# Kernel tuning notes

Hardware: AMD Instinct MI355X
Metric: run time of the kernel (lower is better)

The kernel has to match this reference:

```python
import jax, jax.numpy as jnp
import numpy as np

N_NODES = 100000
N_EDGES = 1600000
IN_C, HID_C, OUT_C = 256, 128, 64


def sage_conv(x, src, dst, Wl, Wr, b, n_nodes):
    """PyG SAGEConv: lin_l(mean of neighbor messages) + lin_r(x) + b."""
    msgs = x[src]  # [E, C] gather
    agg = jax.ops.segment_sum(msgs, dst, num_segments=n_nodes)  # [N, C] scatter-add
    deg = jax.ops.segment_sum(jnp.ones((src.shape[0],), x.dtype), dst, num_segments=n_nodes)
    agg = agg / jnp.maximum(deg, 1.0)[:, None]  # mean aggregation, safe for isolated nodes
    return agg @ Wl + x @ Wr + b


def setup_inputs() -> dict:
    key = jax.random.key(0)
    ks = jax.random.split(key, 12)

    def glorot(k, shape):
        fan_in, fan_out = shape
        lim = float(np.sqrt(6.0 / (fan_in + fan_out)))
        return jax.random.uniform(k, shape, jnp.float32, -lim, lim)

    x = jax.random.normal(ks[0], (N_NODES, IN_C), jnp.float32)
    edge_index = jax.random.randint(ks[1], (2, N_EDGES), 0, N_NODES, jnp.int32)
    return {
        "x": x,
        "edge_index": edge_index,
        "Wl0": glorot(ks[2], (IN_C, HID_C)),
        "Wr0": glorot(ks[3], (IN_C, HID_C)),
        "b0": jnp.zeros((HID_C,), jnp.float32),
        "Wl1": glorot(ks[4], (HID_C, HID_C)),
        "Wr1": glorot(ks[5], (HID_C, HID_C)),
        "b1": jnp.zeros((HID_C,), jnp.float32),
        "Wl2": glorot(ks[6], (HID_C, OUT_C)),
        "Wr2": glorot(ks[7], (HID_C, OUT_C)),
        "b2": jnp.zeros((OUT_C,), jnp.float32),
    }


def reference(x, edge_index, Wl0, Wr0, b0, Wl1, Wr1, b1, Wl2, Wr2, b2):
    src, dst = edge_index[0], edge_index[1]
    n = x.shape[0]
    h = x
    out = None
    # convs[:-1]: conv -> relu -> dropout (eval mode: dropout = identity)
    for Wl, Wr, b in ((Wl0, Wr0, b0), (Wl1, Wr1, b1)):
        out = sage_conv(h, src, dst, Wl, Wr, b, n)
        h = jax.nn.relu(out)
    g = h
    x_final = sage_conv(g, src, dst, Wl2, Wr2, b2, n)
    return (x_final, out, g)
```

## Files before the change

kernel.cpp:

```cpp
#include <hip/hip_runtime.h>
#include <stdint.h>

typedef __attribute__((ext_vector_type(4))) float f32x4;
typedef _Float16 half8 __attribute__((ext_vector_type(8)));
typedef _Float16 half4 __attribute__((ext_vector_type(4)));


#define BIN_CHUNK 8192
#define MAXB 512


template <int K, int NCOLT>
__device__ inline void wprep_one(const float* __restrict__ Wl, const float* __restrict__ Wr,
                                 _Float16* __restrict__ Wt, int i) {
    constexpr int NCOL = NCOLT / 2;
    int n = i / K, k = i - n * K;
    float v = (n < NCOL) ? Wl[(size_t)k * NCOL + n] : Wr[(size_t)k * NCOL + (n - NCOL)];
    Wt[(size_t)(k >> 5) * (NCOLT * 32) + n * 32 + (k & 31)] = (_Float16)v;
}

__global__ __launch_bounds__(256) void k_bhistW(
    const int* __restrict__ dst, int* __restrict__ bcnt, int E, int nbk,
    const float* __restrict__ Wl0, const float* __restrict__ Wr0,
    const float* __restrict__ Wl1, const float* __restrict__ Wr1,
    const float* __restrict__ Wl2, const float* __restrict__ Wr2,
    _Float16* __restrict__ Wt0, _Float16* __restrict__ Wt1, _Float16* __restrict__ Wt2) {
    if ((int)blockIdx.x < nbk) {
        __shared__ int lh[MAXB];
        for (int i = threadIdx.x; i < MAXB; i += 256) lh[i] = 0;
        __syncthreads();
        const int base = blockIdx.x * BIN_CHUNK;
#pragma unroll 4
        for (int i = 0; i < BIN_CHUNK / 256; i++) {
            int e = base + i * 256 + threadIdx.x;
            if (e < E) atomicAdd(&lh[dst[e] >> 8], 1);
        }
        __syncthreads();
        for (int i = threadIdx.x; i < MAXB; i += 256)
            if (lh[i]) atomicAdd(&bcnt[i], lh[i]);
    } else {
        int i = (blockIdx.x - nbk) * 256 + threadIdx.x;
        if (i < 65536) wprep_one<256, 256>(Wl0, Wr0, Wt0, i);
        else if (i < 98304) wprep_one<128, 256>(Wl1, Wr1, Wt1, i - 65536);
        else if (i < 114688) wprep_one<128, 128>(Wl2, Wr2, Wt2, i - 98304);
    }
}

__global__ __launch_bounds__(512) void k_pscan(const int* __restrict__ in,
                                               int* __restrict__ out0,
                                               int* __restrict__ out1,
                                               int* __restrict__ tot, int n) {
    __shared__ int sh[512];
    const int t = threadIdx.x;
    int v[4];
    int s = 0;
#pragma unroll
    for (int i = 0; i < 4; i++) {
        int idx = t * 4 + i;
        v[i] = (idx < n) ? in[idx] : 0;
        s += v[i];
    }
    sh[t] = s;
    __syncthreads();
    for (int off = 1; off < 512; off <<= 1) {
        int add = (t >= off) ? sh[t - off] : 0;
        __syncthreads();
        sh[t] += add;
        __syncthreads();
    }
    int excl = sh[t] - s;
#pragma unroll
    for (int i = 0; i < 4; i++) {
        int idx = t * 4 + i;
        if (idx < n) {
            out0[idx] = excl;
            if (out1) out1[idx] = excl;
        }
        excl += v[i];
    }
    if (t == 511 && tot) *tot = sh[511];
}


__device__ inline void bin_body(const int* __restrict__ src, const int* __restrict__ dst,
                                int* __restrict__ gcur, unsigned* __restrict__ ebuf,
                                int E, int bid, int* __restrict__ smem) {
    int* lh = smem;
    int* lcur = smem + MAXB;
    for (int i = threadIdx.x; i < MAXB; i += 256) lh[i] = 0;
    __syncthreads();
    const int base = bid * BIN_CHUNK;
#pragma unroll 4
    for (int i = 0; i < BIN_CHUNK / 256; i++) {
        int e = base + i * 256 + threadIdx.x;
        if (e < E) atomicAdd(&lh[dst[e] >> 8], 1);
    }
    __syncthreads();
    for (int i = threadIdx.x; i < MAXB; i += 256)
        lcur[i] = lh[i] ? atomicAdd(&gcur[i], lh[i]) : 0;
    __syncthreads();
#pragma unroll 4
    for (int i = 0; i < BIN_CHUNK / 256; i++) {
        int e = base + i * 256 + threadIdx.x;
        if (e < E) {
            int d = dst[e];
            int pos = atomicAdd(&lcur[d >> 8], 1);
            ebuf[pos] = (unsigned)src[e] | ((unsigned)(d & 255) << 24);
        }
    }
}


template <int K, int NCOLT, bool AF32>
__device__ inline void gemm_body(const void* __restrict__ Av,
                                 const _Float16* __restrict__ Wt,
                                 const float* __restrict__ bias,
                                 _Float16* __restrict__ Cl,
                                 _Float16* __restrict__ Cr, int M, int bid,
                                 _Float16* __restrict__ sh) {
    constexpr int NCOL = NCOLT / 2;
    constexpr int WC = NCOLT / 4;
    constexpr int NT = WC / 16;
    constexpr int AS = K + 8;
    constexpr int CS = NCOLT + 8;

    const int tid = threadIdx.x;
    const int lane = tid & 63;
    const int wave = tid >> 6;
    const int quad = lane >> 4;
    const int l16 = lane & 15;
    const int m0 = bid * 64;
    const int colbase = wave * WC;

    if (AF32) {
        const float* A = (const float*)Av;
#pragma unroll
        for (int i = 0; i < K / 16; i++) {
            int off = i * 1024 + tid * 4;
            int row = off / K, col = off % K;
            f32x4 u = {0.f, 0.f, 0.f, 0.f};
            if (m0 + row < M) u = *(const f32x4*)(A + (size_t)(m0 + row) * K + col);
            half4 h = {(_Float16)u[0], (_Float16)u[1], (_Float16)u[2], (_Float16)u[3]};
            *(half4*)(sh + row * AS + col) = h;
        }
    } else {
        const _Float16* A = (const _Float16*)Av;
#pragma unroll
        for (int i = 0; i < K / 32; i++) {
            int off = i * 2048 + tid * 8;
            int row = off / K, col = off % K;
            half8 u = {0, 0, 0, 0, 0, 0, 0, 0};
            if (m0 + row < M) u = *(const half8*)(A + (size_t)(m0 + row) * K + col);
            *(half8*)(sh + row * AS + col) = u;
        }
    }
    __syncthreads();

    f32x4 acc[4][NT];
#pragma unroll
    for (int rg = 0; rg < 4; rg++)
#pragma unroll
        for (int t = 0; t < NT; t++) acc[rg][t] = (f32x4){0.f, 0.f, 0.f, 0.f};

#pragma unroll
    for (int k0 = 0; k0 < K; k0 += 32) {
        half8 a[4];
#pragma unroll
        for (int rg = 0; rg < 4; rg++)
            a[rg] = *(const half8*)(sh + (rg * 16 + l16) * AS + k0 + quad * 8);
        half8 b[NT];
        const _Float16* Wk = Wt + (size_t)(k0 >> 5) * (NCOLT * 32);
#pragma unroll
        for (int t = 0; t < NT; t++)
            b[t] = *(const half8*)(Wk + (colbase + t * 16 + l16) * 32 + quad * 8);
#pragma unroll
        for (int rg = 0; rg < 4; rg++)
#pragma unroll
            for (int t = 0; t < NT; t++)
                acc[rg][t] = __builtin_amdgcn_mfma_f32_16x16x32_f16(b[t], a[rg], acc[rg][t], 0, 0, 0);
    }

    __syncthreads();

#pragma unroll
    for (int t = 0; t < NT; t++) {
        int c0 = colbase + t * 16 + quad * 4;
        f32x4 bv = {0.f, 0.f, 0.f, 0.f};
        if (c0 >= NCOL) bv = *(const f32x4*)(bias + (c0 - NCOL));
#pragma unroll
        for (int rg = 0; rg < 4; rg++) {
            half4 h = {(_Float16)(acc[rg][t][0] + bv[0]), (_Float16)(acc[rg][t][1] + bv[1]),
                       (_Float16)(acc[rg][t][2] + bv[2]), (_Float16)(acc[rg][t][3] + bv[3])};
            *(half4*)(sh + (rg * 16 + l16) * CS + c0) = h;
        }
    }
    __syncthreads();

#pragma unroll
    for (int i = 0; i < (64 * NCOL) / 2048; i++) {
        int off = i * 2048 + tid * 8;
        int row = off / NCOL, col = off % NCOL;
        if (m0 + row < M) {
            *(half8*)(Cl + (size_t)(m0 + row) * NCOL + col) = *(const half8*)(sh + row * CS + col);
            *(half8*)(Cr + (size_t)(m0 + row) * NCOL + col) = *(const half8*)(sh + row * CS + NCOL + col);
        }
    }
}

template <int K, int NCOLT, bool AF32>
__global__ __launch_bounds__(256) void k_gemmM(const void* __restrict__ Av,
                                               const _Float16* __restrict__ Wt,
                                               const float* __restrict__ bias,
                                               _Float16* __restrict__ Cl,
                                               _Float16* __restrict__ Cr, int M) {
    constexpr int MAXS = (K > NCOLT ? K : NCOLT) + 8;
    __shared__ _Float16 sh[64 * MAXS];
    gemm_body<K, NCOLT, AF32>(Av, Wt, bias, Cl, Cr, M, blockIdx.x, sh);
}

__global__ __launch_bounds__(256) void k_binGemm0(
    const int* __restrict__ src, const int* __restrict__ dst,
    int* __restrict__ gcur, unsigned* __restrict__ ebuf, int E, int nbk,
    const float* __restrict__ x, const _Float16* __restrict__ Wt0,
    const float* __restrict__ b0, _Float16* __restrict__ xl,
    _Float16* __restrict__ xr, int M) {
    __shared__ __align__(16) char smem[64 * 264 * 2];
    if ((int)blockIdx.x < nbk) {
        bin_body(src, dst, gcur, ebuf, E, blockIdx.x, (int*)smem);
    } else {
        gemm_body<256, 256, true>(x, Wt0, b0, xl, xr, M, blockIdx.x - nbk,
                                  (_Float16*)smem);
    }
}

__global__ __launch_bounds__(256) void k_csr(const unsigned* __restrict__ ebuf,
                                             const int* __restrict__ bbase,
                                             int* __restrict__ rowptr,
                                             int* __restrict__ ssrc, int N) {
    __shared__ int cnt[256];
    __shared__ int sh[256];
    __shared__ int lc[256];
    const int t = threadIdx.x;
    const int b = blockIdx.x;
    cnt[t] = 0;
    __syncthreads();
    const int lo = bbase[b], hi = bbase[b + 1];
    for (int e = lo + t; e < hi; e += 256)
        atomicAdd(&cnt[ebuf[e] >> 24], 1);
    __syncthreads();
    const int myc = cnt[t];
    sh[t] = myc;
    __syncthreads();
    for (int off = 1; off < 256; off <<= 1) {
        int add = (t >= off) ? sh[t - off] : 0;
        __syncthreads();
        sh[t] += add;
        __syncthreads();
    }
    const int base = lo + (sh[t] - myc);
    const int n = (b << 8) + t;
    if (n <= N) rowptr[n] = base;
    lc[t] = base;
    __syncthreads();
    for (int e = lo + t; e < hi; e += 256) {
        unsigned v = ebuf[e];
        int pos = atomicAdd(&lc[v >> 24], 1);
        ssrc[pos] = (int)(v & 0xFFFFFFu);
    }
}


template <int COUT, int MODE>
__global__ __launch_bounds__(256) void k_agg(const half8* __restrict__ xl,
                                             const half8* __restrict__ xr,
                                             const int* __restrict__ rowptr,
                                             const int* __restrict__ ssrc,
                                             float* __restrict__ outF1,
                                             float* __restrict__ outF2,
                                             _Float16* __restrict__ outH, int N) {
    constexpr int LPN = COUT / 16;
    constexpr int NPB = 256 / LPN;
    constexpr int C8 = COUT / 8;
    const int tid = threadIdx.x;
    const int c = tid % LPN;
    const int n = blockIdx.x * NPB + tid / LPN;
    if (n >= N) return;

    const int rp0 = rowptr[n];
    const int rp1 = rowptr[n + 1];
    float acc[16];
#pragma unroll
    for (int i = 0; i < 16; i++) acc[i] = 0.f;

    const size_t cb = (size_t)c * 2;
    int e = rp0;
    for (; e + 3 < rp1; e += 4) {
        int s0 = ssrc[e], s1 = ssrc[e + 1], s2 = ssrc[e + 2], s3 = ssrc[e + 3];
        half8 v0a = xl[(size_t)s0 * C8 + cb], v0b = xl[(size_t)s0 * C8 + cb + 1];
        half8 v1a = xl[(size_t)s1 * C8 + cb], v1b = xl[(size_t)s1 * C8 + cb + 1];
        half8 v2a = xl[(size_t)s2 * C8 + cb], v2b = xl[(size_t)s2 * C8 + cb + 1];
        half8 v3a = xl[(size_t)s3 * C8 + cb], v3b = xl[(size_t)s3 * C8 + cb + 1];
#pragma unroll
        for (int i = 0; i < 8; i++) {
            acc[i] += (float)v0a[i] + (float)v1a[i] + (float)v2a[i] + (float)v3a[i];
            acc[8 + i] += (float)v0b[i] + (float)v1b[i] + (float)v2b[i] + (float)v3b[i];
        }
    }
    for (; e < rp1; e++) {
        int s = ssrc[e];
        half8 va = xl[(size_t)s * C8 + cb], vb = xl[(size_t)s * C8 + cb + 1];
#pragma unroll
        for (int i = 0; i < 8; i++) {
            acc[i] += (float)va[i];
            acc[8 + i] += (float)vb[i];
        }
    }

    const int deg = rp1 - rp0;
    const float scale = 1.0f / (float)(deg > 1 ? deg : 1);
    half8 x0 = xr[(size_t)n * C8 + cb];
    half8 x1 = xr[(size_t)n * C8 + cb + 1];
    float res[16];
#pragma unroll
    for (int i = 0; i < 8; i++) {
        res[i] = acc[i] * scale + (float)x0[i];
        res[8 + i] = acc[8 + i] * scale + (float)x1[i];
    }

    const size_t ob = (size_t)n * COUT + (size_t)c * 16;
    if (MODE == 0) {
        half8 h0v, h1v;
#pragma unroll
        for (int i = 0; i < 8; i++) {
            h0v[i] = (_Float16)(res[i] > 0.f ? res[i] : 0.f);
            h1v[i] = (_Float16)(res[8 + i] > 0.f ? res[8 + i] : 0.f);
        }
        *(half8*)(outH + ob) = h0v;
        *(half8*)(outH + ob + 8) = h1v;
    } else if (MODE == 1) {
#pragma unroll
        for (int q = 0; q < 4; q++) {
            f32x4 v = {res[q * 4], res[q * 4 + 1], res[q * 4 + 2], res[q * 4 + 3]};
            *(f32x4*)(outF1 + ob + q * 4) = v;
            f32x4 z = {v[0] > 0.f ? v[0] : 0.f, v[1] > 0.f ? v[1] : 0.f,
                       v[2] > 0.f ? v[2] : 0.f, v[3] > 0.f ? v[3] : 0.f};
            *(f32x4*)(outF2 + ob + q * 4) = z;
        }
        half8 h0v, h1v;
#pragma unroll
        for (int i = 0; i < 8; i++) {
            h0v[i] = (_Float16)(res[i] > 0.f ? res[i] : 0.f);
            h1v[i] = (_Float16)(res[8 + i] > 0.f ? res[8 + i] : 0.f);
        }
        *(half8*)(outH + ob) = h0v;
        *(half8*)(outH + ob + 8) = h1v;
    } else {
#pragma unroll
        for (int q = 0; q < 4; q++) {
            f32x4 v = {res[q * 4], res[q * 4 + 1], res[q * 4 + 2], res[q * 4 + 3]};
            *(f32x4*)(outF1 + ob + q * 4) = v;
        }
    }
}


extern "C" void kernel_launch(void* const* d_in, const int* in_sizes, int n_in,
                              void* d_out, int out_size, void* d_ws, size_t ws_size,
                              hipStream_t stream) {
    const float* x   = (const float*)d_in[0];
    const int*   ei  = (const int*)d_in[1];
    const float* Wl0 = (const float*)d_in[2];
    const float* Wr0 = (const float*)d_in[3];
    const float* b0  = (const float*)d_in[4];
    const float* Wl1 = (const float*)d_in[5];
    const float* Wr1 = (const float*)d_in[6];
    const float* b1  = (const float*)d_in[7];
    const float* Wl2 = (const float*)d_in[8];
    const float* Wr2 = (const float*)d_in[9];
    const float* b2  = (const float*)d_in[10];

    const int N = in_sizes[0] / 256;
    const int E = in_sizes[1] / 2;
    const int* src = ei;
    const int* dst = ei + E;

    char* p = (char*)d_ws;
    auto alloc = [&](size_t bytes) -> void* {
        void* r = (void*)p;
        p += (bytes + 255) & ~(size_t)255;
        return r;
    };
    int*      rowptr   = (int*)alloc((size_t)(N + 1) * 4);
    int*      bcnt     = (int*)alloc(MAXB * 4);
    int*      bbase    = (int*)alloc((MAXB + 1) * 4);
    int*      gcur     = (int*)alloc(MAXB * 4);
    int*      ssrc     = (int*)alloc((size_t)E * 4);
    _Float16* xl       = (_Float16*)alloc((size_t)N * 128 * 2);
    _Float16* xr       = (_Float16*)alloc((size_t)N * 128 * 2);
    _Float16* h0       = (_Float16*)alloc((size_t)N * 128 * 2);
    _Float16* gb       = (_Float16*)alloc((size_t)N * 128 * 2);
    _Float16* Wt0      = (_Float16*)alloc((size_t)256 * 256 * 2);
    _Float16* Wt1      = (_Float16*)alloc((size_t)256 * 128 * 2);
    _Float16* Wt2      = (_Float16*)alloc((size_t)128 * 128 * 2);

    unsigned* ebuf = (unsigned*)gb;

    float* out = (float*)d_out;
    float* x_final = out;
    float* out1    = out + (size_t)N * 64;
    float* g       = out + (size_t)N * 192;

    const int nb = (N + 255) >> 8;
    const int nbk = (E + BIN_CHUNK - 1) / BIN_CHUNK;
    const int gGrid = (N + 63) / 64;

    hipMemsetAsync(bcnt, 0, MAXB * 4, stream);
    k_bhistW<<<nbk + 448, 256, 0, stream>>>(dst, bcnt, E, nbk,
                                            Wl0, Wr0, Wl1, Wr1, Wl2, Wr2,
                                            Wt0, Wt1, Wt2);
    k_pscan<<<1, 512, 0, stream>>>(bcnt, bbase, gcur, bbase + nb, nb);
    k_binGemm0<<<nbk + gGrid, 256, 0, stream>>>(src, dst, gcur, ebuf, E, nbk,
                                                x, Wt0, b0, xl, xr, N);
    k_csr<<<nb, 256, 0, stream>>>(ebuf, bbase, rowptr, ssrc, N);

    k_agg<128, 0><<<(N + 31) / 32, 256, 0, stream>>>((const half8*)xl, (const half8*)xr,
                                                     rowptr, ssrc, nullptr, nullptr, h0, N);

    k_gemmM<128, 256, false><<<gGrid, 256, 0, stream>>>(h0, Wt1, b1, xl, xr, N);
    k_agg<128, 1><<<(N + 31) / 32, 256, 0, stream>>>((const half8*)xl, (const half8*)xr,
                                                     rowptr, ssrc, out1, g, gb, N);

    k_gemmM<128, 128, false><<<gGrid, 256, 0, stream>>>(gb, Wt2, b2, xl, xr, N);
    k_agg<64, 2><<<(N + 63) / 64, 256, 0, stream>>>((const half8*)xl, (const half8*)xr,
                                                    rowptr, ssrc, x_final, nullptr, nullptr, N);
}
```

Before: 513.6 us.

## Fuse neighbor aggregation with following layer GEMM via shared memory

Combines the mean-aggregation kernel of layers 0 and 1 with the next layer's dense transform. Each block aggregates 64 node rows into LDS as fp16 and then runs the MFMA GEMM on that tile, so the h0 and gb intermediates are never written to or re-read from global memory. The cost is ping-pong xl/xr buffers instead of in-place reuse, and a lower-occupancy combined kernel. Each block also waits on its aggregation before starting the GEMM, so gather latency and matrix work can no longer run as separate full-width kernels.

```diff
diff --git a/kernel.cpp b/kernel.cpp
--- a/kernel.cpp
+++ b/kernel.cpp
@@ -111,6 +111,77 @@
 }
 
 
+template <int K, int NCOLT>
+__device__ inline void gemm_core(_Float16* __restrict__ sh,
+                                 const _Float16* __restrict__ Wt,
+                                 const float* __restrict__ bias,
+                                 _Float16* __restrict__ Cl,
+                                 _Float16* __restrict__ Cr, int M, int bid) {
+    constexpr int NCOL = NCOLT / 2;
+    constexpr int WC = NCOLT / 4;
+    constexpr int NT = WC / 16;
+    constexpr int AS = K + 8;
+    constexpr int CS = NCOLT + 8;
+
+    const int tid = threadIdx.x;
+    const int lane = tid & 63;
+    const int wave = tid >> 6;
+    const int quad = lane >> 4;
+    const int l16 = lane & 15;
+    const int m0 = bid * 64;
+    const int colbase = wave * WC;
+
+    f32x4 acc[4][NT];
+#pragma unroll
+    for (int rg = 0; rg < 4; rg++)
+#pragma unroll
+        for (int t = 0; t < NT; t++) acc[rg][t] = (f32x4){0.f, 0.f, 0.f, 0.f};
+
+#pragma unroll
+    for (int k0 = 0; k0 < K; k0 += 32) {
+        half8 a[4];
+#pragma unroll
+        for (int rg = 0; rg < 4; rg++)
+            a[rg] = *(const half8*)(sh + (rg * 16 + l16) * AS + k0 + quad * 8);
+        half8 b[NT];
+        const _Float16* Wk = Wt + (size_t)(k0 >> 5) * (NCOLT * 32);
+#pragma unroll
+        for (int t = 0; t < NT; t++)
+            b[t] = *(const half8*)(Wk + (colbase + t * 16 + l16) * 32 + quad * 8);
+#pragma unroll
+        for (int rg = 0; rg < 4; rg++)
+#pragma unroll
+            for (int t = 0; t < NT; t++)
+                acc[rg][t] = __builtin_amdgcn_mfma_f32_16x16x32_f16(b[t], a[rg], acc[rg][t], 0, 0, 0);
+    }
+
+    __syncthreads();
+
+#pragma unroll
+    for (int t = 0; t < NT; t++) {
+        int c0 = colbase + t * 16 + quad * 4;
+        f32x4 bv = {0.f, 0.f, 0.f, 0.f};
+        if (c0 >= NCOL) bv = *(const f32x4*)(bias + (c0 - NCOL));
+#pragma unroll
+        for (int rg = 0; rg < 4; rg++) {
+            half4 h = {(_Float16)(acc[rg][t][0] + bv[0]), (_Float16)(acc[rg][t][1] + bv[1]),
+                       (_Float16)(acc[rg][t][2] + bv[2]), (_Float16)(acc[rg][t][3] + bv[3])};
+            *(half4*)(sh + (rg * 16 + l16) * CS + c0) = h;
+        }
+    }
+    __syncthreads();
+
+#pragma unroll
+    for (int i = 0; i < (64 * NCOL) / 2048; i++) {
+        int off = i * 2048 + tid * 8;
+        int row = off / NCOL, col = off % NCOL;
+        if (m0 + row < M) {
+            *(half8*)(Cl + (size_t)(m0 + row) * NCOL + col) = *(const half8*)(sh + row * CS + col);
+            *(half8*)(Cr + (size_t)(m0 + row) * NCOL + col) = *(const half8*)(sh + row * CS + NCOL + col);
+        }
+    }
+}
+
 template <int K, int NCOLT, bool AF32>
 __device__ inline void gemm_body(const void* __restrict__ Av,
                                  const _Float16* __restrict__ Wt,
@@ -118,19 +189,9 @@
                                  _Float16* __restrict__ Cl,
                                  _Float16* __restrict__ Cr, int M, int bid,
                                  _Float16* __restrict__ sh) {
-    constexpr int NCOL = NCOLT / 2;
-    constexpr int WC = NCOLT / 4;
-    constexpr int NT = WC / 16;
     constexpr int AS = K + 8;
-    constexpr int CS = NCOLT + 8;
-
     const int tid = threadIdx.x;
-    const int lane = tid & 63;
-    const int wave = tid >> 6;
-    const int quad = lane >> 4;
-    const int l16 = lane & 15;
     const int m0 = bid * 64;
-    const int colbase = wave * WC;
 
     if (AF32) {
         const float* A = (const float*)Av;
@@ -155,67 +216,7 @@
         }
     }
     __syncthreads();
-
-    f32x4 acc[4][NT];
-#pragma unroll
-    for (int rg = 0; rg < 4; rg++)
-#pragma unroll
-        for (int t = 0; t < NT; t++) acc[rg][t] = (f32x4){0.f, 0.f, 0.f, 0.f};
-
-#pragma unroll
-    for (int k0 = 0; k0 < K; k0 += 32) {
-        half8 a[4];
-#pragma unroll
-        for (int rg = 0; rg < 4; rg++)
-            a[rg] = *(const half8*)(sh + (rg * 16 + l16) * AS + k0 + quad * 8);
-        half8 b[NT];
-        const _Float16* Wk = Wt + (size_t)(k0 >> 5) * (NCOLT * 32);
-#pragma unroll
-        for (int t = 0; t < NT; t++)
-            b[t] = *(const half8*)(Wk + (colbase + t * 16 + l16) * 32 + quad * 8);
-#pragma unroll
-        for (int rg = 0; rg < 4; rg++)
-#pragma unroll
-            for (int t = 0; t < NT; t++)
-                acc[rg][t] = __builtin_amdgcn_mfma_f32_16x16x32_f16(b[t], a[rg], acc[rg][t], 0, 0, 0);
-    }
-
-    __syncthreads();
-
-#pragma unroll
-    for (int t = 0; t < NT; t++) {
-        int c0 = colbase + t * 16 + quad * 4;
-        f32x4 bv = {0.f, 0.f, 0.f, 0.f};
-        if (c0 >= NCOL) bv = *(const f32x4*)(bias + (c0 - NCOL));
-#pragma unroll
-        for (int rg = 0; rg < 4; rg++) {
-            half4 h = {(_Float16)(acc[rg][t][0] + bv[0]), (_Float16)(acc[rg][t][1] + bv[1]),
-                       (_Float16)(acc[rg][t][2] + bv[2]), (_Float16)(acc[rg][t][3] + bv[3])};
-            *(half4*)(sh + (rg * 16 + l16) * CS + c0) = h;
-        }
-    }
-    __syncthreads();
-
-#pragma unroll
-    for (int i = 0; i < (64 * NCOL) / 2048; i++) {
-        int off = i * 2048 + tid * 8;
-        int row = off / NCOL, col = off % NCOL;
-        if (m0 + row < M) {
-            *(half8*)(Cl + (size_t)(m0 + row) * NCOL + col) = *(const half8*)(sh + row * CS + col);
-            *(half8*)(Cr + (size_t)(m0 + row) * NCOL + col) = *(const half8*)(sh + row * CS + NCOL + col);
-        }
-    }
-}
-
-template <int K, int NCOLT, bool AF32>
-__global__ __launch_bounds__(256) void k_gemmM(const void* __restrict__ Av,
-                                               const _Float16* __restrict__ Wt,
-                                               const float* __restrict__ bias,
-                                               _Float16* __restrict__ Cl,
-                                               _Float16* __restrict__ Cr, int M) {
-    constexpr int MAXS = (K > NCOLT ? K : NCOLT) + 8;
-    __shared__ _Float16 sh[64 * MAXS];
-    gemm_body<K, NCOLT, AF32>(Av, Wt, bias, Cl, Cr, M, blockIdx.x, sh);
+    gemm_core<K, NCOLT>(sh, Wt, bias, Cl, Cr, M, bid);
 }
 
 __global__ __launch_bounds__(256) void k_binGemm0(
@@ -267,6 +268,97 @@
         int pos = atomicAdd(&lc[v >> 24], 1);
         ssrc[pos] = (int)(v & 0xFFFFFFu);
     }
+}
+
+
+template <int NCOLT, int MODE>
+__global__ __launch_bounds__(256) void k_aggGemm(
+    const half8* __restrict__ xin_l, const half8* __restrict__ xin_r,
+    const int* __restrict__ rowptr, const int* __restrict__ ssrc,
+    float* __restrict__ outF1, float* __restrict__ outF2,
+    const _Float16* __restrict__ Wt, const float* __restrict__ bias,
+    _Float16* __restrict__ Cl, _Float16* __restrict__ Cr, int N) {
+    constexpr int K = 128;
+    constexpr int AS = K + 8;
+    constexpr int MAXS = (NCOLT > K ? NCOLT : K) + 8;
+    __shared__ _Float16 sh[64 * MAXS];
+
+    const int tid = threadIdx.x;
+    const int m0 = blockIdx.x * 64;
+    const int c = tid & 7;
+    const int gidx = tid >> 3;
+    const size_t cb = (size_t)c * 2;
+
+#pragma unroll 1
+    for (int sub = 0; sub < 2; sub++) {
+        const int row = sub * 32 + gidx;
+        const int n = m0 + row;
+        half8 h0v = {0, 0, 0, 0, 0, 0, 0, 0};
+        half8 h1v = {0, 0, 0, 0, 0, 0, 0, 0};
+        if (n < N) {
+            const int rp0 = rowptr[n];
+            const int rp1 = rowptr[n + 1];
+            float acc[16];
+#pragma unroll
+            for (int i = 0; i < 16; i++) acc[i] = 0.f;
+
+            int e = rp0;
+            for (; e + 3 < rp1; e += 4) {
+                int s0 = ssrc[e], s1 = ssrc[e + 1], s2 = ssrc[e + 2], s3 = ssrc[e + 3];
+                half8 v0a = xin_l[(size_t)s0 * 16 + cb], v0b = xin_l[(size_t)s0 * 16 + cb + 1];
+                half8 v1a = xin_l[(size_t)s1 * 16 + cb], v1b = xin_l[(size_t)s1 * 16 + cb + 1];
+                half8 v2a = xin_l[(size_t)s2 * 16 + cb], v2b = xin_l[(size_t)s2 * 16 + cb + 1];
+                half8 v3a = xin_l[(size_t)s3 * 16 + cb], v3b = xin_l[(size_t)s3 * 16 + cb + 1];
+#pragma unroll
+                for (int i = 0; i < 8; i++) {
+                    acc[i] += (float)v0a[i] + (float)v1a[i] + (float)v2a[i] + (float)v3a[i];
+                    acc[8 + i] += (float)v0b[i] + (float)v1b[i] + (float)v2b[i] + (float)v3b[i];
+                }
+            }
+            for (; e < rp1; e++) {
+                int s = ssrc[e];
+                half8 va = xin_l[(size_t)s * 16 + cb], vb = xin_l[(size_t)s * 16 + cb + 1];
+#pragma unroll
+                for (int i = 0; i < 8; i++) {
+                    acc[i] += (float)va[i];
+                    acc[8 + i] += (float)vb[i];
+                }
+            }
+
+            const int deg = rp1 - rp0;
+            const float scale = 1.0f / (float)(deg > 1 ? deg : 1);
+            half8 x0 = xin_r[(size_t)n * 16 + cb];
+            half8 x1 = xin_r[(size_t)n * 16 + cb + 1];
+            float res[16];
+#pragma unroll
+            for (int i = 0; i < 8; i++) {
+                res[i] = acc[i] * scale + (float)x0[i];
+                res[8 + i] = acc[8 + i] * scale + (float)x1[i];
+            }
+
+            if (MODE == 1) {
+                const size_t ob = (size_t)n * 128 + (size_t)c * 16;
+#pragma unroll
+                for (int q = 0; q < 4; q++) {
+                    f32x4 v = {res[q * 4], res[q * 4 + 1], res[q * 4 + 2], res[q * 4 + 3]};
+                    *(f32x4*)(outF1 + ob + q * 4) = v;
+                    f32x4 z = {v[0] > 0.f ? v[0] : 0.f, v[1] > 0.f ? v[1] : 0.f,
+                               v[2] > 0.f ? v[2] : 0.f, v[3] > 0.f ? v[3] : 0.f};
+                    *(f32x4*)(outF2 + ob + q * 4) = z;
+                }
+            }
+#pragma unroll
+            for (int i = 0; i < 8; i++) {
+                h0v[i] = (_Float16)(res[i] > 0.f ? res[i] : 0.f);
+                h1v[i] = (_Float16)(res[8 + i] > 0.f ? res[8 + i] : 0.f);
+            }
+        }
+        *(half8*)(sh + row * AS + c * 16) = h0v;
+        *(half8*)(sh + row * AS + c * 16 + 8) = h1v;
+    }
+    __syncthreads();
+
+    gemm_core<K, NCOLT>(sh, Wt, bias, Cl, Cr, N, blockIdx.x);
 }
 
 
@@ -328,33 +420,7 @@
     }
 
     const size_t ob = (size_t)n * COUT + (size_t)c * 16;
-    if (MODE == 0) {
-        half8 h0v, h1v;
-#pragma unroll
-        for (int i = 0; i < 8; i++) {
-            h0v[i] = (_Float16)(res[i] > 0.f ? res[i] : 0.f);
-            h1v[i] = (_Float16)(res[8 + i] > 0.f ? res[8 + i] : 0.f);
-        }
-        *(half8*)(outH + ob) = h0v;
-        *(half8*)(outH + ob + 8) = h1v;
-    } else if (MODE == 1) {
-#pragma unroll
-        for (int q = 0; q < 4; q++) {
-            f32x4 v = {res[q * 4], res[q * 4 + 1], res[q * 4 + 2], res[q * 4 + 3]};
-            *(f32x4*)(outF1 + ob + q * 4) = v;
-            f32x4 z = {v[0] > 0.f ? v[0] : 0.f, v[1] > 0.f ? v[1] : 0.f,
-                       v[2] > 0.f ? v[2] : 0.f, v[3] > 0.f ? v[3] : 0.f};
-            *(f32x4*)(outF2 + ob + q * 4) = z;
-        }
-        half8 h0v, h1v;
-#pragma unroll
-        for (int i = 0; i < 8; i++) {
-            h0v[i] = (_Float16)(res[i] > 0.f ? res[i] : 0.f);
-            h1v[i] = (_Float16)(res[8 + i] > 0.f ? res[8 + i] : 0.f);
-        }
-        *(half8*)(outH + ob) = h0v;
-        *(half8*)(outH + ob + 8) = h1v;
-    } else {
+    if (MODE == 2) {
 #pragma unroll
         for (int q = 0; q < 4; q++) {
             f32x4 v = {res[q * 4], res[q * 4 + 1], res[q * 4 + 2], res[q * 4 + 3]};
@@ -397,13 +463,13 @@
     int*      ssrc     = (int*)alloc((size_t)E * 4);
     _Float16* xl       = (_Float16*)alloc((size_t)N * 128 * 2);
     _Float16* xr       = (_Float16*)alloc((size_t)N * 128 * 2);
-    _Float16* h0       = (_Float16*)alloc((size_t)N * 128 * 2);
-    _Float16* gb       = (_Float16*)alloc((size_t)N * 128 * 2);
+    _Float16* xl2      = (_Float16*)alloc((size_t)N * 128 * 2);
+    _Float16* xr2      = (_Float16*)alloc((size_t)N * 128 * 2);
     _Float16* Wt0      = (_Float16*)alloc((size_t)256 * 256 * 2);
     _Float16* Wt1      = (_Float16*)alloc((size_t)256 * 128 * 2);
     _Float16* Wt2      = (_Float16*)alloc((size_t)128 * 128 * 2);
 
-    unsigned* ebuf = (unsigned*)gb;
+    unsigned* ebuf = (unsigned*)xl2;
 
     float* out = (float*)d_out;
     float* x_final = out;
@@ -423,14 +489,14 @@
                                                 x, Wt0, b0, xl, xr, N);
     k_csr<<<nb, 256, 0, stream>>>(ebuf, bbase, rowptr, ssrc, N);
 
-    k_agg<128, 0><<<(N + 31) / 32, 256, 0, stream>>>((const half8*)xl, (const half8*)xr,
-                                                     rowptr, ssrc, nullptr, nullptr, h0, N);
-
-    k_gemmM<128, 256, false><<<gGrid, 256, 0, stream>>>(h0, Wt1, b1, xl, xr, N);
-    k_agg<128, 1><<<(N + 31) / 32, 256, 0, stream>>>((const half8*)xl, (const half8*)xr,
-                                                     rowptr, ssrc, out1, g, gb, N);
-
-    k_gemmM<128, 128, false><<<gGrid, 256, 0, stream>>>(gb, Wt2, b2, xl, xr, N);
+    k_aggGemm<256, 0><<<gGrid, 256, 0, stream>>>((const half8*)xl, (const half8*)xr,
+                                                 rowptr, ssrc, nullptr, nullptr,
+                                                 Wt1, b1, xl2, xr2, N);
+
+    k_aggGemm<128, 1><<<gGrid, 256, 0, stream>>>((const half8*)xl2, (const half8*)xr2,
+                                                 rowptr, ssrc, out1, g,
+                                                 Wt2, b2, xl, xr, N);
+
     k_agg<64, 2><<<(N + 63) / 64, 256, 0, stream>>>((const half8*)xl, (const half8*)xr,
                                                     rowptr, ssrc, x_final, nullptr, nullptr, N);
 }
```

Result: faster. 502.7 us (-2.1%).
